# Kernel tuning notes

Measured on AMD Instinct MI355X. Metric: run time of the kernel, lower is better.

## Reference

```python
import jax, jax.numpy as jnp
import numpy as np

BATCH = 16384
IN_F = 1024
OUT_F = 1024
NUM_BASIS = 8
DEGREE = 3
K = NUM_BASIS + DEGREE  # 11 basis columns
EPS = 1e-5


def _knots():
    return jnp.linspace(0.0, 1.0, K + 1)


def _compute_basis(x):
    """Cox-de Boor recursion, faithful to the torch in-place variant:
    at degree d only columns j < K-d are updated; higher columns keep
    their lower-degree values (and are still contracted in the einsum).
    x: [B, IN_F] -> basis: [B, IN_F, K]
    """
    knots = _knots().astype(x.dtype)
    xa = x[..., None]  # [B, IN_F, 1]
    # degree-0 indicator: x in [knots[j], knots[j+1])
    basis = ((xa >= knots[:K]) & (xa < knots[1:K + 1])).astype(x.dtype)
    for d in range(1, DEGREE + 1):
        m = K - d
        denom1 = knots[d:K] - knots[:m]            # [m]
        denom2 = knots[d + 1:K + 1] - knots[1:m + 1]  # [m]
        safe1 = jnp.where(denom1 != 0, denom1, 1.0)
        safe2 = jnp.where(denom2 != 0, denom2, 1.0)
        alpha = jnp.where(denom1 != 0, (xa - knots[:m]) / safe1, 0.0)
        beta = jnp.where(denom2 != 0, (knots[d + 1:K + 1] - xa) / safe2, 0.0)
        new = alpha * basis[..., :m] + beta * basis[..., 1:m + 1]
        basis = jnp.concatenate([new, basis[..., m:]], axis=-1)
    return basis


def setup_inputs() -> dict:
    key = jax.random.key(0)
    k1, k2, k3, k4 = jax.random.split(key, 4)
    x = jax.random.uniform(k1, (BATCH, IN_F), dtype=jnp.float32)
    # Xavier-uniform control points [out, in, K]
    bound_cp = float(np.sqrt(6.0 / (IN_F + K)))  # torch xavier treats last dims as fan
    control_points = jax.random.uniform(k2, (OUT_F, IN_F, K), minval=-bound_cp, maxval=bound_cp, dtype=jnp.float32)
    bound_w = float(np.sqrt(6.0 / (IN_F + OUT_F)))
    W = jax.random.uniform(k3, (OUT_F, IN_F), minval=-bound_w, maxval=bound_w, dtype=jnp.float32)
    b = jnp.zeros((OUT_F,), dtype=jnp.float32)
    gamma = jnp.ones((OUT_F,), dtype=jnp.float32)
    beta = jnp.zeros((OUT_F,), dtype=jnp.float32)
    return {"x": x, "control_points": control_points, "W": W, "b": b,
            "gamma": gamma, "beta": beta}


def reference(x, control_points, W, b, gamma, beta):
    basis = _compute_basis(x)  # [B, IN_F, K]
    spline_out = jnp.einsum('bik,oik->bo', basis, control_points)  # [B, OUT_F]
    out = spline_out + x @ W.T + b
    # LayerNorm over last dim (dropout is identity in eval / p used as 0)
    mu = jnp.mean(out, axis=-1, keepdims=True)
    var = jnp.mean(jnp.square(out - mu), axis=-1, keepdims=True)
    return gamma * (out - mu) * jax.lax.rsqrt(var + EPS) + beta
```

## Files before the change

kernel.cpp:

```cpp
#include <hip/hip_runtime.h>
#include <hip/hip_bf16.h>

#define BATCH   16384
#define IN_F    1024
#define OUT_F   1024
#define KCOLS   11
#define KPL     12
#define KP      (KPL*IN_F)
#define KHALF   (KP/2)
#define NTKH    (KHALF/64)
#define NITH    (NTKH/2)
#define LN_EPS  1e-5f

typedef __attribute__((ext_vector_type(8))) short short8;
typedef __attribute__((ext_vector_type(4))) float f32x4;

static __device__ __forceinline__ unsigned short f2bf(float f) {
  __hip_bfloat16 h = __float2bfloat16(f);
  return *reinterpret_cast<unsigned short*>(&h);
}

__device__ __forceinline__ void bspline_basis(float x, float bas[KCOLS]) {
  const float s = 1.0f / 11.0f;
  float kn[12];
#pragma unroll
  for (int j = 0; j < 12; ++j) kn[j] = (float)j * s;
  kn[11] = 1.0f;
#pragma unroll
  for (int j = 0; j < 11; ++j)
    bas[j] = (x >= kn[j] && x < kn[j + 1]) ? 1.0f : 0.0f;
#pragma unroll
  for (int d = 1; d <= 3; ++d) {
#pragma unroll
    for (int j = 0; j < 11 - d; ++j) {
      const float r1 = 1.0f / (kn[j + d] - kn[j]);
      const float r2 = 1.0f / (kn[j + d + 1] - kn[j + 1]);
      float a = (x - kn[j]) * r1;
      float c = (kn[j + d + 1] - x) * r2;
      bas[j] = a * bas[j] + c * bas[j + 1];
    }
  }
}

__global__ __launch_bounds__(256) void featgen(const float* __restrict__ X,
                                               unsigned short* __restrict__ A,
                                               int row0) {
  const int brow = blockIdx.x;
  const int i0 = threadIdx.x * 4;
  const float4 xv = *reinterpret_cast<const float4*>(X + (size_t)(row0 + brow) * IN_F + i0);
  float xs[4] = {xv.x, xv.y, xv.z, xv.w};
  float bas[4][KCOLS];
#pragma unroll
  for (int t = 0; t < 4; ++t) bspline_basis(xs[t], bas[t]);
  unsigned short* outp = A + (size_t)brow * KP + i0;
#pragma unroll
  for (int k = 0; k < KCOLS; ++k) {
    ushort4 u;
    u.x = f2bf(bas[0][k]); u.y = f2bf(bas[1][k]);
    u.z = f2bf(bas[2][k]); u.w = f2bf(bas[3][k]);
    *reinterpret_cast<ushort4*>(outp + (size_t)k * IN_F) = u;
  }
  ushort4 u;
  u.x = f2bf(xs[0]); u.y = f2bf(xs[1]); u.z = f2bf(xs[2]); u.w = f2bf(xs[3]);
  *reinterpret_cast<ushort4*>(outp + (size_t)KCOLS * IN_F) = u;
}

__global__ __launch_bounds__(256) void bgen(const float* __restrict__ CP,
                                            const float* __restrict__ W,
                                            unsigned short* __restrict__ Bm) {
  const int o = blockIdx.x;
  const int i0 = threadIdx.x * 4;
  unsigned short* outp = Bm + (size_t)o * KP + i0;
#pragma unroll
  for (int k = 0; k < KCOLS; ++k) {
    ushort4 u;
    u.x = f2bf(CP[((size_t)o * IN_F + i0 + 0) * KCOLS + k]);
    u.y = f2bf(CP[((size_t)o * IN_F + i0 + 1) * KCOLS + k]);
    u.z = f2bf(CP[((size_t)o * IN_F + i0 + 2) * KCOLS + k]);
    u.w = f2bf(CP[((size_t)o * IN_F + i0 + 3) * KCOLS + k]);
    *reinterpret_cast<ushort4*>(outp + (size_t)k * IN_F) = u;
  }
  ushort4 u;
  u.x = f2bf(W[(size_t)o * IN_F + i0 + 0]);
  u.y = f2bf(W[(size_t)o * IN_F + i0 + 1]);
  u.z = f2bf(W[(size_t)o * IN_F + i0 + 2]);
  u.w = f2bf(W[(size_t)o * IN_F + i0 + 3]);
  *reinterpret_cast<ushort4*>(outp + (size_t)KCOLS * IN_F) = u;
}


#define BAR()    __builtin_amdgcn_s_barrier()
#define SCHED0() __builtin_amdgcn_sched_barrier(0)
#define WAITV(N) asm volatile("s_waitcnt vmcnt(" #N ")" ::: "memory")

__global__ __launch_bounds__(512, 2) void gemm8p(const unsigned short* __restrict__ A,
                                                 const unsigned short* __restrict__ Bm,
                                                 float* __restrict__ Cc,
                                                 float* __restrict__ Cp, int nbm) {
  __shared__ unsigned short lds[2][2][2][128 * 64];
  const int tid  = (int)threadIdx.x;
  const int lane = tid & 63;
  const int w    = tid >> 6;
  const int wm   = w >> 2;
  const int wn   = w & 3;

  const int nwg = nbm * 8;
  const int cpx = nwg >> 3;
  const int bid = (int)blockIdx.x;
  const int swz = (bid & 7) * cpx + (bid >> 3);
  const int bn = swz & 3;
  const int ks = (swz >> 2) & 1;
  const int bm = swz >> 3;
  const size_t koff = (size_t)ks * KHALF;
  float* __restrict__ C = ks ? Cp : Cc;

  const int srow = (w << 3) + (lane >> 3);
  const int scol = ((lane & 7) ^ (lane >> 3)) << 3;
  const unsigned short* aB = A  + (size_t)(bm * 256 + srow) * KP + koff + scol;
  const unsigned short* bB = Bm + (size_t)(bn * 256 + srow) * KP + koff + scol;

#define STAGE(T, AB, H, BUF)                                                          \
  do {                                                                                \
    if ((T) < NTKH) {                                                                 \
      const unsigned short* g_ = ((AB) ? bB : aB) + (size_t)(H) * 128 * KP + (size_t)(T) * 64; \
      unsigned short* l_ = &lds[BUF][AB][H][w * 512];                                 \
      __builtin_amdgcn_global_load_lds((const __attribute__((address_space(1))) void*)g_,       \
                                       (__attribute__((address_space(3))) void*)l_, 16, 0, 0);  \
      __builtin_amdgcn_global_load_lds((const __attribute__((address_space(1))) void*)(g_ + (size_t)64 * KP), \
                                       (__attribute__((address_space(3))) void*)(l_ + 4096), 16, 0, 0); \
    }                                                                                 \
  } while (0)

  const int fr = lane & 15;
  const int g4 = lane >> 4;
  const int s7 = lane & 7;
  const int col0 = ((g4 ^ s7) << 3);
  const int col1 = (((4 + g4) ^ s7) << 3);
  const unsigned short* aH[2] = {&lds[0][0][wm][0], &lds[1][0][wm][0]};
  const unsigned short* bH[2] = {&lds[0][1][wn >> 1][0], &lds[1][1][wn >> 1][0]};
  const int brow0 = (wn & 1) * 64;

  short8 aF[4][2], bF0[2][2], bF1[2][2];
  f32x4 acc[8][4] = {};

#define LOADA(MB, BUF)                                                         \
  do {                                                                         \
    _Pragma("unroll") for (int m_ = 0; m_ < 4; ++m_) {                         \
      const unsigned short* p_ = aH[BUF] + ((MB) + m_) * 1024 + fr * 64;       \
      aF[m_][0] = *reinterpret_cast<const short8*>(p_ + col0);                 \
      aF[m_][1] = *reinterpret_cast<const short8*>(p_ + col1);                 \
    }                                                                          \
  } while (0)

#define LOADB(DST, NB, BUF)                                                    \
  do {                                                                         \
    _Pragma("unroll") for (int n_ = 0; n_ < 2; ++n_) {                         \
      const unsigned short* p_ = bH[BUF] + (brow0 + ((NB) + n_) * 16 + fr) * 64; \
      DST[n_][0] = *reinterpret_cast<const short8*>(p_ + col0);                \
      DST[n_][1] = *reinterpret_cast<const short8*>(p_ + col1);                \
    }                                                                          \
  } while (0)

#define MFMAQ(MB, NB, BF)                                                      \
  do {                                                                         \
    __builtin_amdgcn_s_setprio(1);                                             \
    _Pragma("unroll") for (int m_ = 0; m_ < 4; ++m_)                           \
    _Pragma("unroll") for (int n_ = 0; n_ < 2; ++n_)                           \
    _Pragma("unroll") for (int kk_ = 0; kk_ < 2; ++kk_)                        \
      acc[(MB) + m_][(NB) + n_] = __builtin_amdgcn_mfma_f32_16x16x32_bf16(     \
          aF[m_][kk_], BF[n_][kk_], acc[(MB) + m_][(NB) + n_], 0, 0, 0);       \
    __builtin_amdgcn_s_setprio(0);                                             \
  } while (0)

  STAGE(0, 1, 0, 0); STAGE(0, 1, 1, 0);
  STAGE(0, 0, 0, 0); STAGE(0, 0, 1, 0);
  STAGE(1, 1, 0, 1); STAGE(1, 1, 1, 1);
  WAITV(4);
  BAR();

#pragma unroll 1
  for (int j = 0; j < NITH; ++j) {
    const int tA = 2 * j + 1, tB2 = 2 * j + 2, tB3 = 2 * j + 3;
    LOADA(0, 0); LOADB(bF0, 0, 0);
    STAGE(tA, 0, 0, 1);
    MFMAQ(0, 0, bF0);
    SCHED0(); BAR();
    LOADB(bF1, 2, 0);
    STAGE(tA, 0, 1, 1);
    MFMAQ(0, 2, bF1);
    SCHED0(); BAR();
    LOADA(4, 0);
    STAGE(tB2, 1, 0, 0);
    MFMAQ(4, 0, bF0);
    SCHED0(); BAR();
    STAGE(tB2, 1, 1, 0);
    MFMAQ(4, 2, bF1);
    if (j < NITH - 1) { WAITV(4); } else { WAITV(0); }
    SCHED0(); BAR();
    LOADA(0, 1); LOADB(bF0, 0, 1);
    STAGE(tB2, 0, 0, 0);
    MFMAQ(0, 0, bF0);
    SCHED0(); BAR();
    LOADB(bF1, 2, 1);
    STAGE(tB2, 0, 1, 0);
    MFMAQ(0, 2, bF1);
    SCHED0(); BAR();
    LOADA(4, 1);
    STAGE(tB3, 1, 0, 1);
    MFMAQ(4, 0, bF0);
    SCHED0(); BAR();
    STAGE(tB3, 1, 1, 1);
    MFMAQ(4, 2, bF1);
    if (j < NITH - 1) { WAITV(4); }
    SCHED0(); BAR();
  }

  const size_t r0 = (size_t)bm * 256 + wm * 128 + (lane >> 4) * 4;
  const int c0 = bn * 256 + wn * 64 + fr;
#pragma unroll
  for (int m = 0; m < 8; ++m)
#pragma unroll
    for (int n = 0; n < 4; ++n)
#pragma unroll
      for (int r = 0; r < 4; ++r)
        C[(r0 + m * 16 + r) * OUT_F + (c0 + n * 16)] = acc[m][n][r];
}

__global__ __launch_bounds__(256) void ln_kernel(float* __restrict__ C,
                                                 const float* __restrict__ P,
                                                 const float* __restrict__ bias,
                                                 const float* __restrict__ gamma,
                                                 const float* __restrict__ beta) {
  const int row = blockIdx.x;
  const int tid = threadIdx.x;
  float4 v = *reinterpret_cast<const float4*>(C + (size_t)row * OUT_F + tid * 4);
  const float4 p = *reinterpret_cast<const float4*>(P + (size_t)row * OUT_F + tid * 4);
  const float4 bb = *reinterpret_cast<const float4*>(bias + tid * 4);
  v.x += p.x + bb.x; v.y += p.y + bb.y; v.z += p.z + bb.z; v.w += p.w + bb.w;
  float s = v.x + v.y + v.z + v.w;
  float q = v.x * v.x + v.y * v.y + v.z * v.z + v.w * v.w;
#pragma unroll
  for (int off = 32; off > 0; off >>= 1) {
    s += __shfl_down(s, off);
    q += __shfl_down(q, off);
  }
  __shared__ float red[8];
  const int wave = tid >> 6, lane = tid & 63;
  if (lane == 0) { red[wave] = s; red[4 + wave] = q; }
  __syncthreads();
  s = red[0] + red[1] + red[2] + red[3];
  q = red[4] + red[5] + red[6] + red[7];
  const float mu = s * (1.0f / OUT_F);
  const float var = q * (1.0f / OUT_F) - mu * mu;
  const float rs = rsqrtf(var + LN_EPS);
  const float4 g = *reinterpret_cast<const float4*>(gamma + tid * 4);
  const float4 be = *reinterpret_cast<const float4*>(beta + tid * 4);
  float4 o;
  o.x = g.x * (v.x - mu) * rs + be.x;
  o.y = g.y * (v.y - mu) * rs + be.y;
  o.z = g.z * (v.z - mu) * rs + be.z;
  o.w = g.w * (v.w - mu) * rs + be.w;
  *reinterpret_cast<float4*>(C + (size_t)row * OUT_F + tid * 4) = o;
}

extern "C" void kernel_launch(void* const* d_in, const int* in_sizes, int n_in,
                              void* d_out, int out_size, void* d_ws, size_t ws_size,
                              hipStream_t stream) {
  const float* x     = (const float*)d_in[0];
  const float* cp    = (const float*)d_in[1];
  const float* W     = (const float*)d_in[2];
  const float* bias  = (const float*)d_in[3];
  const float* gamma = (const float*)d_in[4];
  const float* beta  = (const float*)d_in[5];
  float* out = (float*)d_out;

  unsigned short* Bm = (unsigned short*)d_ws;
  const size_t bBytes = (size_t)OUT_F * KP * sizeof(unsigned short);
  size_t avail = ws_size > bBytes ? ws_size - bBytes : 0;
  const size_t perRow = (size_t)KP * 2 + (size_t)OUT_F * 4;
  long long fit = (long long)(avail / perRow);
  int chunk;
  if (fit >= BATCH)     chunk = BATCH;
  else if (fit >= 8192) chunk = 8192;
  else                  chunk = (int)((fit / 256) * 256);
  if (chunk < 256) chunk = 256;

  unsigned short* Af = (unsigned short*)((char*)d_ws + bBytes);
  float* P = (float*)(Af + (size_t)chunk * KP);

  bgen<<<OUT_F, 256, 0, stream>>>(cp, W, Bm);
  for (int r0 = 0; r0 < BATCH; r0 += chunk) {
    const int rows = (BATCH - r0 < chunk) ? (BATCH - r0) : chunk;
    featgen<<<rows, 256, 0, stream>>>(x, Af, r0);
    const int nbm = rows / 256;
    gemm8p<<<nbm * 8, 512, 0, stream>>>(Af, Bm, out + (size_t)r0 * OUT_F, P, nbm);
    ln_kernel<<<rows, 256, 0, stream>>>(out + (size_t)r0 * OUT_F, P, bias, gamma, beta);
  }
}
```

Measured before the change: 442.3 us.

## Pre-pack B in MFMA fragment order and load it directly from global

The weight/control-point matrix is now packed by a new bgen2 kernel into a layout that matches the per-lane MFMA B-fragment order. The GEMM loads B fragments straight from global memory into registers, so only A is staged through LDS, which halves shared-memory usage and LDS traffic. The cost is more global/L2 reads of B per workgroup with no LDS sharing across waves, and the pipeline wait counts had to be retuned, which may expose load latency.

```diff
diff --git a/kernel.cpp b/kernel.cpp
--- a/kernel.cpp
+++ b/kernel.cpp
@@ -65,27 +65,34 @@
   *reinterpret_cast<ushort4*>(outp + (size_t)KCOLS * IN_F) = u;
 }
 
-__global__ __launch_bounds__(256) void bgen(const float* __restrict__ CP,
-                                            const float* __restrict__ W,
-                                            unsigned short* __restrict__ Bm) {
-  const int o = blockIdx.x;
-  const int i0 = threadIdx.x * 4;
-  unsigned short* outp = Bm + (size_t)o * KP + i0;
-#pragma unroll
-  for (int k = 0; k < KCOLS; ++k) {
-    ushort4 u;
-    u.x = f2bf(CP[((size_t)o * IN_F + i0 + 0) * KCOLS + k]);
-    u.y = f2bf(CP[((size_t)o * IN_F + i0 + 1) * KCOLS + k]);
-    u.z = f2bf(CP[((size_t)o * IN_F + i0 + 2) * KCOLS + k]);
-    u.w = f2bf(CP[((size_t)o * IN_F + i0 + 3) * KCOLS + k]);
-    *reinterpret_cast<ushort4*>(outp + (size_t)k * IN_F) = u;
-  }
-  ushort4 u;
-  u.x = f2bf(W[(size_t)o * IN_F + i0 + 0]);
-  u.y = f2bf(W[(size_t)o * IN_F + i0 + 1]);
-  u.z = f2bf(W[(size_t)o * IN_F + i0 + 2]);
-  u.w = f2bf(W[(size_t)o * IN_F + i0 + 3]);
-  *reinterpret_cast<ushort4*>(outp + (size_t)KCOLS * IN_F) = u;
+__global__ __launch_bounds__(256) void bgen2(const float* __restrict__ CP,
+                                             const float* __restrict__ W,
+                                             unsigned short* __restrict__ BP) {
+  const int bx = blockIdx.x;
+  const int bn = bx / (16 * 96);
+  const int rem = bx % (16 * 96);
+  const int ob = rem / 96;
+  const int tgg = rem % 96;
+  const int tid = threadIdx.x;
+  const int lane = tid & 63;
+  const int kk = (tid >> 6) & 1;
+  const int ts = tid >> 7;
+  const int tg = tgg * 2 + ts;
+  const int fr = lane & 15;
+  const int g4 = lane >> 4;
+  const int o = bn * 256 + ob * 16 + fr;
+  const int k0 = tg * 64 + kk * 32 + g4 * 8;
+  const int p = k0 >> 10;
+  const int i0 = k0 & 1023;
+  unsigned short v[8];
+#pragma unroll
+  for (int e = 0; e < 8; ++e) {
+    float f = (p < KCOLS) ? CP[((size_t)o * IN_F + i0 + e) * KCOLS + p]
+                          : W[(size_t)o * IN_F + i0 + e];
+    v[e] = f2bf(f);
+  }
+  unsigned short* dst = BP + (size_t)tg * 65536 + bn * 16384 + ob * 1024 + kk * 512 + lane * 8;
+  *reinterpret_cast<short8*>(dst) = *reinterpret_cast<short8*>(v);
 }
 
 
@@ -94,10 +101,10 @@
 #define WAITV(N) asm volatile("s_waitcnt vmcnt(" #N ")" ::: "memory")
 
 __global__ __launch_bounds__(512, 2) void gemm8p(const unsigned short* __restrict__ A,
-                                                 const unsigned short* __restrict__ Bm,
+                                                 const unsigned short* __restrict__ BP,
                                                  float* __restrict__ Cc,
                                                  float* __restrict__ Cp, int nbm) {
-  __shared__ unsigned short lds[2][2][2][128 * 64];
+  __shared__ unsigned short lds[2][256 * 64];
   const int tid  = (int)threadIdx.x;
   const int lane = tid & 63;
   const int w    = tid >> 6;
@@ -116,18 +123,14 @@
 
   const int srow = (w << 3) + (lane >> 3);
   const int scol = ((lane & 7) ^ (lane >> 3)) << 3;
-  const unsigned short* aB = A  + (size_t)(bm * 256 + srow) * KP + koff + scol;
-  const unsigned short* bB = Bm + (size_t)(bn * 256 + srow) * KP + koff + scol;
-
-#define STAGE(T, AB, H, BUF)                                                          \
+  const unsigned short* aB = A + (size_t)(bm * 256 + srow) * KP + koff + scol;
+
+#define STAGE_A(T, ISS, BUF)                                                          \
   do {                                                                                \
     if ((T) < NTKH) {                                                                 \
-      const unsigned short* g_ = ((AB) ? bB : aB) + (size_t)(H) * 128 * KP + (size_t)(T) * 64; \
-      unsigned short* l_ = &lds[BUF][AB][H][w * 512];                                 \
-      __builtin_amdgcn_global_load_lds((const __attribute__((address_space(1))) void*)g_,       \
-                                       (__attribute__((address_space(3))) void*)l_, 16, 0, 0);  \
-      __builtin_amdgcn_global_load_lds((const __attribute__((address_space(1))) void*)(g_ + (size_t)64 * KP), \
-                                       (__attribute__((address_space(3))) void*)(l_ + 4096), 16, 0, 0); \
+      const unsigned short* g_ = aB + (size_t)(ISS) * 64 * KP + (size_t)(T) * 64;     \
+      __builtin_amdgcn_global_load_lds((const __attribute__((address_space(1))) void*)g_, \
+          (__attribute__((address_space(3))) void*)(&lds[BUF][(ISS) * 4096 + w * 512]), 16, 0, 0); \
     }                                                                                 \
   } while (0)
 
@@ -136,9 +139,17 @@
   const int s7 = lane & 7;
   const int col0 = ((g4 ^ s7) << 3);
   const int col1 = (((4 + g4) ^ s7) << 3);
-  const unsigned short* aH[2] = {&lds[0][0][wm][0], &lds[1][0][wm][0]};
-  const unsigned short* bH[2] = {&lds[0][1][wn >> 1][0], &lds[1][1][wn >> 1][0]};
-  const int brow0 = (wn & 1) * 64;
+
+  const unsigned short* bpT = BP + (size_t)(ks * NTKH) * 65536 +
+                              (size_t)bn * 16384 + (size_t)wn * 4096 + (size_t)lane * 8;
+
+#define LOADB_G(DST, NB, TG)                                                   \
+  do {                                                                         \
+    const unsigned short* q_ = bpT + (size_t)(TG) * 65536;                     \
+    _Pragma("unroll") for (int n_ = 0; n_ < 2; ++n_)                           \
+    _Pragma("unroll") for (int kk_ = 0; kk_ < 2; ++kk_)                        \
+      DST[n_][kk_] = *reinterpret_cast<const short8*>(q_ + ((NB) + n_) * 1024 + kk_ * 512); \
+  } while (0)
 
   short8 aF[4][2], bF0[2][2], bF1[2][2];
   f32x4 acc[8][4] = {};
@@ -146,18 +157,9 @@
 #define LOADA(MB, BUF)                                                         \
   do {                                                                         \
     _Pragma("unroll") for (int m_ = 0; m_ < 4; ++m_) {                         \
-      const unsigned short* p_ = aH[BUF] + ((MB) + m_) * 1024 + fr * 64;       \
+      const unsigned short* p_ = &lds[BUF][(wm * 128 + ((MB) + m_) * 16 + fr) * 64]; \
       aF[m_][0] = *reinterpret_cast<const short8*>(p_ + col0);                 \
       aF[m_][1] = *reinterpret_cast<const short8*>(p_ + col1);                 \
-    }                                                                          \
-  } while (0)
-
-#define LOADB(DST, NB, BUF)                                                    \
-  do {                                                                         \
-    _Pragma("unroll") for (int n_ = 0; n_ < 2; ++n_) {                         \
-      const unsigned short* p_ = bH[BUF] + (brow0 + ((NB) + n_) * 16 + fr) * 64; \
-      DST[n_][0] = *reinterpret_cast<const short8*>(p_ + col0);                \
-      DST[n_][1] = *reinterpret_cast<const short8*>(p_ + col1);                \
     }                                                                          \
   } while (0)
 
@@ -172,46 +174,49 @@
     __builtin_amdgcn_s_setprio(0);                                             \
   } while (0)
 
-  STAGE(0, 1, 0, 0); STAGE(0, 1, 1, 0);
-  STAGE(0, 0, 0, 0); STAGE(0, 0, 1, 0);
-  STAGE(1, 1, 0, 1); STAGE(1, 1, 1, 1);
-  WAITV(4);
+  STAGE_A(0, 0, 0); STAGE_A(0, 1, 0); STAGE_A(0, 2, 0); STAGE_A(0, 3, 0);
+  STAGE_A(1, 0, 1);
+  LOADB_G(bF0, 0, 0);
+  WAITV(5);
   BAR();
 
 #pragma unroll 1
   for (int j = 0; j < NITH; ++j) {
-    const int tA = 2 * j + 1, tB2 = 2 * j + 2, tB3 = 2 * j + 3;
-    LOADA(0, 0); LOADB(bF0, 0, 0);
-    STAGE(tA, 0, 0, 1);
+    const int ta = 2 * j, tb = 2 * j + 1;
+    const int tgn = (2 * j + 2 < NTKH) ? 2 * j + 2 : NTKH - 1;
+    LOADA(0, 0);
+    LOADB_G(bF1, 2, ta);
+    STAGE_A(tb, 1, 1);
     MFMAQ(0, 0, bF0);
     SCHED0(); BAR();
-    LOADB(bF1, 2, 0);
-    STAGE(tA, 0, 1, 1);
+    STAGE_A(tb, 2, 1);
     MFMAQ(0, 2, bF1);
     SCHED0(); BAR();
     LOADA(4, 0);
-    STAGE(tB2, 1, 0, 0);
+    STAGE_A(tb, 3, 1);
     MFMAQ(4, 0, bF0);
     SCHED0(); BAR();
-    STAGE(tB2, 1, 1, 0);
+    LOADB_G(bF0, 0, tb);
+    STAGE_A(ta + 2, 0, 0);
     MFMAQ(4, 2, bF1);
-    if (j < NITH - 1) { WAITV(4); } else { WAITV(0); }
-    SCHED0(); BAR();
-    LOADA(0, 1); LOADB(bF0, 0, 1);
-    STAGE(tB2, 0, 0, 0);
+    if (j < NITH - 1) { WAITV(5); } else { WAITV(0); }
+    SCHED0(); BAR();
+    LOADA(0, 1);
+    LOADB_G(bF1, 2, tb);
+    STAGE_A(ta + 2, 1, 0);
     MFMAQ(0, 0, bF0);
     SCHED0(); BAR();
-    LOADB(bF1, 2, 1);
-    STAGE(tB2, 0, 1, 0);
+    STAGE_A(ta + 2, 2, 0);
     MFMAQ(0, 2, bF1);
     SCHED0(); BAR();
     LOADA(4, 1);
-    STAGE(tB3, 1, 0, 1);
+    STAGE_A(ta + 2, 3, 0);
     MFMAQ(4, 0, bF0);
     SCHED0(); BAR();
-    STAGE(tB3, 1, 1, 1);
+    LOADB_G(bF0, 0, tgn);
+    STAGE_A(ta + 3, 0, 1);
     MFMAQ(4, 2, bF1);
-    if (j < NITH - 1) { WAITV(4); }
+    if (j < NITH - 1) { WAITV(5); }
     SCHED0(); BAR();
   }
 
@@ -274,7 +279,7 @@
   const float* beta  = (const float*)d_in[5];
   float* out = (float*)d_out;
 
-  unsigned short* Bm = (unsigned short*)d_ws;
+  unsigned short* BP = (unsigned short*)d_ws;
   const size_t bBytes = (size_t)OUT_F * KP * sizeof(unsigned short);
   size_t avail = ws_size > bBytes ? ws_size - bBytes : 0;
   const size_t perRow = (size_t)KP * 2 + (size_t)OUT_F * 4;
@@ -288,12 +293,12 @@
   unsigned short* Af = (unsigned short*)((char*)d_ws + bBytes);
   float* P = (float*)(Af + (size_t)chunk * KP);
 
-  bgen<<<OUT_F, 256, 0, stream>>>(cp, W, Bm);
+  bgen2<<<4 * 16 * 96, 256, 0, stream>>>(cp, W, BP);
   for (int r0 = 0; r0 < BATCH; r0 += chunk) {
     const int rows = (BATCH - r0 < chunk) ? (BATCH - r0) : chunk;
     featgen<<<rows, 256, 0, stream>>>(x, Af, r0);
     const int nbm = rows / 256;
-    gemm8p<<<nbm * 8, 512, 0, stream>>>(Af, Bm, out + (size_t)r0 * OUT_F, P, nbm);
+    gemm8p<<<nbm * 8, 512, 0, stream>>>(Af, BP, out + (size_t)r0 * OUT_F, P, nbm);
     ln_kernel<<<rows, 256, 0, stream>>>(out + (size_t)r0 * OUT_F, P, bias, gamma, beta);
   }
 }
```

Result: slower. 602.5 us (+36.2%).

## Double-buffer A fragments and software-pipeline LDS reads ahead of MFMAs

Applied to the files above, without the earlier changes.

Adds a second register set for A fragments so LDS reads for the next quadrant are issued one phase ahead of the MFMAs that consume them. The main loop's stage and wait ordering changes, with vmcnt waits moved and relaxed from 4 to 2. The aim is to hide LDS read latency behind matrix math. In exchange it uses more VGPRs, which could lower occupancy, and the reordered waits and barriers carry a risk of races on buffer reuse.

```diff
diff --git a/kernel.cpp b/kernel.cpp
--- a/kernel.cpp
+++ b/kernel.cpp
@@ -140,15 +140,15 @@
   const unsigned short* bH[2] = {&lds[0][1][wn >> 1][0], &lds[1][1][wn >> 1][0]};
   const int brow0 = (wn & 1) * 64;
 
-  short8 aF[4][2], bF0[2][2], bF1[2][2];
+  short8 aFA[4][2], aFB[4][2], bF0[2][2], bF1[2][2];
   f32x4 acc[8][4] = {};
 
-#define LOADA(MB, BUF)                                                         \
+#define LOADA_D(DST, MB, BUF)                                                  \
   do {                                                                         \
     _Pragma("unroll") for (int m_ = 0; m_ < 4; ++m_) {                         \
       const unsigned short* p_ = aH[BUF] + ((MB) + m_) * 1024 + fr * 64;       \
-      aF[m_][0] = *reinterpret_cast<const short8*>(p_ + col0);                 \
-      aF[m_][1] = *reinterpret_cast<const short8*>(p_ + col1);                 \
+      DST[m_][0] = *reinterpret_cast<const short8*>(p_ + col0);                \
+      DST[m_][1] = *reinterpret_cast<const short8*>(p_ + col1);                \
     }                                                                          \
   } while (0)
 
@@ -161,57 +161,61 @@
     }                                                                          \
   } while (0)
 
-#define MFMAQ(MB, NB, BF)                                                      \
+#define MFMAQ_D(AFR, MB, NB, BF)                                               \
   do {                                                                         \
     __builtin_amdgcn_s_setprio(1);                                             \
     _Pragma("unroll") for (int m_ = 0; m_ < 4; ++m_)                           \
     _Pragma("unroll") for (int n_ = 0; n_ < 2; ++n_)                           \
     _Pragma("unroll") for (int kk_ = 0; kk_ < 2; ++kk_)                        \
       acc[(MB) + m_][(NB) + n_] = __builtin_amdgcn_mfma_f32_16x16x32_bf16(     \
-          aF[m_][kk_], BF[n_][kk_], acc[(MB) + m_][(NB) + n_], 0, 0, 0);       \
+          AFR[m_][kk_], BF[n_][kk_], acc[(MB) + m_][(NB) + n_], 0, 0, 0);      \
     __builtin_amdgcn_s_setprio(0);                                             \
   } while (0)
 
+  STAGE(0, 0, 0, 0); STAGE(0, 0, 1, 0);
   STAGE(0, 1, 0, 0); STAGE(0, 1, 1, 0);
-  STAGE(0, 0, 0, 0); STAGE(0, 0, 1, 0);
   STAGE(1, 1, 0, 1); STAGE(1, 1, 1, 1);
   WAITV(4);
   BAR();
+  LOADA_D(aFA, 0, 0);
+  LOADB(bF0, 0, 0);
 
 #pragma unroll 1
   for (int j = 0; j < NITH; ++j) {
-    const int tA = 2 * j + 1, tB2 = 2 * j + 2, tB3 = 2 * j + 3;
-    LOADA(0, 0); LOADB(bF0, 0, 0);
-    STAGE(tA, 0, 0, 1);
-    MFMAQ(0, 0, bF0);
-    SCHED0(); BAR();
+    const int tb = 2 * j + 1, t2 = 2 * j + 2, t3 = 2 * j + 3;
     LOADB(bF1, 2, 0);
-    STAGE(tA, 0, 1, 1);
-    MFMAQ(0, 2, bF1);
-    SCHED0(); BAR();
-    LOADA(4, 0);
-    STAGE(tB2, 1, 0, 0);
-    MFMAQ(4, 0, bF0);
-    SCHED0(); BAR();
-    STAGE(tB2, 1, 1, 0);
-    MFMAQ(4, 2, bF1);
-    if (j < NITH - 1) { WAITV(4); } else { WAITV(0); }
-    SCHED0(); BAR();
-    LOADA(0, 1); LOADB(bF0, 0, 1);
-    STAGE(tB2, 0, 0, 0);
-    MFMAQ(0, 0, bF0);
+    STAGE(tb, 0, 0, 1);
+    MFMAQ_D(aFA, 0, 0, bF0);
+    SCHED0(); BAR();
+    LOADA_D(aFB, 4, 0);
+    STAGE(tb, 0, 1, 1);
+    MFMAQ_D(aFA, 0, 2, bF1);
+    SCHED0(); BAR();
+    STAGE(t2, 1, 0, 0);
+    MFMAQ_D(aFB, 4, 0, bF0);
+    if (j < NITH - 1) { WAITV(2); } else { WAITV(0); }
+    SCHED0(); BAR();
+    LOADA_D(aFA, 0, 1);
+    LOADB(bF0, 0, 1);
+    STAGE(t2, 1, 1, 0);
+    MFMAQ_D(aFB, 4, 2, bF1);
     SCHED0(); BAR();
     LOADB(bF1, 2, 1);
-    STAGE(tB2, 0, 1, 0);
-    MFMAQ(0, 2, bF1);
-    SCHED0(); BAR();
-    LOADA(4, 1);
-    STAGE(tB3, 1, 0, 1);
-    MFMAQ(4, 0, bF0);
-    SCHED0(); BAR();
-    STAGE(tB3, 1, 1, 1);
-    MFMAQ(4, 2, bF1);
-    if (j < NITH - 1) { WAITV(4); }
+    STAGE(t2, 0, 0, 0);
+    MFMAQ_D(aFA, 0, 0, bF0);
+    SCHED0(); BAR();
+    LOADA_D(aFB, 4, 1);
+    STAGE(t2, 0, 1, 0);
+    MFMAQ_D(aFA, 0, 2, bF1);
+    SCHED0(); BAR();
+    STAGE(t3, 1, 0, 1);
+    MFMAQ_D(aFB, 4, 0, bF0);
+    if (j < NITH - 1) { WAITV(2); } else { WAITV(0); }
+    SCHED0(); BAR();
+    LOADA_D(aFA, 0, 0);
+    LOADB(bF0, 0, 0);
+    STAGE(t3, 1, 1, 1);
+    MFMAQ_D(aFB, 4, 2, bF1);
     SCHED0(); BAR();
   }
 
```

After: 476.9 us. +7.8%, slower.

## Store split-K GEMM partials as bf16 and widen featgen stores to 16 bytes

Applied to the files above, without the earlier changes.

The GEMM now writes both split-K partial results as bf16 into workspace buffers instead of fp32 into the output and a partial buffer. The LayerNorm kernel reads the two bf16 partials, sums them with the bias and writes fp32 output. This halves partial-result traffic between the GEMM and LayerNorm. Separately, featgen processes 8 features per thread with 16-byte stores, and the GEMM prologue stage order is swapped. The bf16 rounding of the partial sums before normalization reduces accuracy.

```diff
diff --git a/kernel.cpp b/kernel.cpp
--- a/kernel.cpp
+++ b/kernel.cpp
@@ -19,6 +19,10 @@
   __hip_bfloat16 h = __float2bfloat16(f);
   return *reinterpret_cast<unsigned short*>(&h);
 }
+static __device__ __forceinline__ float bf2f(unsigned short u) {
+  unsigned int x = ((unsigned int)u) << 16;
+  return *reinterpret_cast<float*>(&x);
+}
 
 __device__ __forceinline__ void bspline_basis(float x, float bas[KCOLS]) {
   const float s = 1.0f / 11.0f;
@@ -45,24 +49,27 @@
 __global__ __launch_bounds__(256) void featgen(const float* __restrict__ X,
                                                unsigned short* __restrict__ A,
                                                int row0) {
-  const int brow = blockIdx.x;
-  const int i0 = threadIdx.x * 4;
-  const float4 xv = *reinterpret_cast<const float4*>(X + (size_t)(row0 + brow) * IN_F + i0);
-  float xs[4] = {xv.x, xv.y, xv.z, xv.w};
-  float bas[4][KCOLS];
-#pragma unroll
-  for (int t = 0; t < 4; ++t) bspline_basis(xs[t], bas[t]);
+  const int tid = threadIdx.x;
+  const int brow = blockIdx.x * 2 + (tid >> 7);
+  const int i0 = (tid & 127) * 8;
+  const float4 xv0 = *reinterpret_cast<const float4*>(X + (size_t)(row0 + brow) * IN_F + i0);
+  const float4 xv1 = *reinterpret_cast<const float4*>(X + (size_t)(row0 + brow) * IN_F + i0 + 4);
+  float xs[8] = {xv0.x, xv0.y, xv0.z, xv0.w, xv1.x, xv1.y, xv1.z, xv1.w};
+  float bas[8][KCOLS];
+#pragma unroll
+  for (int t = 0; t < 8; ++t) bspline_basis(xs[t], bas[t]);
   unsigned short* outp = A + (size_t)brow * KP + i0;
 #pragma unroll
   for (int k = 0; k < KCOLS; ++k) {
-    ushort4 u;
-    u.x = f2bf(bas[0][k]); u.y = f2bf(bas[1][k]);
-    u.z = f2bf(bas[2][k]); u.w = f2bf(bas[3][k]);
-    *reinterpret_cast<ushort4*>(outp + (size_t)k * IN_F) = u;
-  }
-  ushort4 u;
-  u.x = f2bf(xs[0]); u.y = f2bf(xs[1]); u.z = f2bf(xs[2]); u.w = f2bf(xs[3]);
-  *reinterpret_cast<ushort4*>(outp + (size_t)KCOLS * IN_F) = u;
+    unsigned short u[8];
+#pragma unroll
+    for (int t = 0; t < 8; ++t) u[t] = f2bf(bas[t][k]);
+    *reinterpret_cast<short8*>(outp + (size_t)k * IN_F) = *reinterpret_cast<short8*>(u);
+  }
+  unsigned short u[8];
+#pragma unroll
+  for (int t = 0; t < 8; ++t) u[t] = f2bf(xs[t]);
+  *reinterpret_cast<short8*>(outp + (size_t)KCOLS * IN_F) = *reinterpret_cast<short8*>(u);
 }
 
 __global__ __launch_bounds__(256) void bgen(const float* __restrict__ CP,
@@ -95,8 +102,8 @@
 
 __global__ __launch_bounds__(512, 2) void gemm8p(const unsigned short* __restrict__ A,
                                                  const unsigned short* __restrict__ Bm,
-                                                 float* __restrict__ Cc,
-                                                 float* __restrict__ Cp, int nbm) {
+                                                 unsigned short* __restrict__ Cb0,
+                                                 unsigned short* __restrict__ Cb1, int nbm) {
   __shared__ unsigned short lds[2][2][2][128 * 64];
   const int tid  = (int)threadIdx.x;
   const int lane = tid & 63;
@@ -112,7 +119,7 @@
   const int ks = (swz >> 2) & 1;
   const int bm = swz >> 3;
   const size_t koff = (size_t)ks * KHALF;
-  float* __restrict__ C = ks ? Cp : Cc;
+  unsigned short* __restrict__ C = ks ? Cb1 : Cb0;
 
   const int srow = (w << 3) + (lane >> 3);
   const int scol = ((lane & 7) ^ (lane >> 3)) << 3;
@@ -172,8 +179,8 @@
     __builtin_amdgcn_s_setprio(0);                                             \
   } while (0)
 
+  STAGE(0, 0, 0, 0); STAGE(0, 0, 1, 0);
   STAGE(0, 1, 0, 0); STAGE(0, 1, 1, 0);
-  STAGE(0, 0, 0, 0); STAGE(0, 0, 1, 0);
   STAGE(1, 1, 0, 1); STAGE(1, 1, 1, 1);
   WAITV(4);
   BAR();
@@ -223,20 +230,25 @@
     for (int n = 0; n < 4; ++n)
 #pragma unroll
       for (int r = 0; r < 4; ++r)
-        C[(r0 + m * 16 + r) * OUT_F + (c0 + n * 16)] = acc[m][n][r];
-}
-
-__global__ __launch_bounds__(256) void ln_kernel(float* __restrict__ C,
-                                                 const float* __restrict__ P,
+        C[(r0 + m * 16 + r) * OUT_F + (c0 + n * 16)] = f2bf(acc[m][n][r]);
+}
+
+__global__ __launch_bounds__(256) void ln_kernel(const unsigned short* __restrict__ C0,
+                                                 const unsigned short* __restrict__ C1,
+                                                 float* __restrict__ Out,
                                                  const float* __restrict__ bias,
                                                  const float* __restrict__ gamma,
                                                  const float* __restrict__ beta) {
   const int row = blockIdx.x;
   const int tid = threadIdx.x;
-  float4 v = *reinterpret_cast<const float4*>(C + (size_t)row * OUT_F + tid * 4);
-  const float4 p = *reinterpret_cast<const float4*>(P + (size_t)row * OUT_F + tid * 4);
+  const ushort4 a = *reinterpret_cast<const ushort4*>(C0 + (size_t)row * OUT_F + tid * 4);
+  const ushort4 b = *reinterpret_cast<const ushort4*>(C1 + (size_t)row * OUT_F + tid * 4);
   const float4 bb = *reinterpret_cast<const float4*>(bias + tid * 4);
-  v.x += p.x + bb.x; v.y += p.y + bb.y; v.z += p.z + bb.z; v.w += p.w + bb.w;
+  float4 v;
+  v.x = bf2f(a.x) + bf2f(b.x) + bb.x;
+  v.y = bf2f(a.y) + bf2f(b.y) + bb.y;
+  v.z = bf2f(a.z) + bf2f(b.z) + bb.z;
+  v.w = bf2f(a.w) + bf2f(b.w) + bb.w;
   float s = v.x + v.y + v.z + v.w;
   float q = v.x * v.x + v.y * v.y + v.z * v.z + v.w * v.w;
 #pragma unroll
@@ -260,7 +272,7 @@
   o.y = g.y * (v.y - mu) * rs + be.y;
   o.z = g.z * (v.z - mu) * rs + be.z;
   o.w = g.w * (v.w - mu) * rs + be.w;
-  *reinterpret_cast<float4*>(C + (size_t)row * OUT_F + tid * 4) = o;
+  *reinterpret_cast<float4*>(Out + (size_t)row * OUT_F + tid * 4) = o;
 }
 
 extern "C" void kernel_launch(void* const* d_in, const int* in_sizes, int n_in,
@@ -285,15 +297,17 @@
   else                  chunk = (int)((fit / 256) * 256);
   if (chunk < 256) chunk = 256;
 
-  unsigned short* Af = (unsigned short*)((char*)d_ws + bBytes);
-  float* P = (float*)(Af + (size_t)chunk * KP);
+  unsigned short* Af  = (unsigned short*)((char*)d_ws + bBytes);
+  unsigned short* Cb0 = Af + (size_t)chunk * KP;
+  unsigned short* Cb1 = Cb0 + (size_t)chunk * OUT_F;
 
   bgen<<<OUT_F, 256, 0, stream>>>(cp, W, Bm);
   for (int r0 = 0; r0 < BATCH; r0 += chunk) {
     const int rows = (BATCH - r0 < chunk) ? (BATCH - r0) : chunk;
-    featgen<<<rows, 256, 0, stream>>>(x, Af, r0);
+    featgen<<<rows / 2, 256, 0, stream>>>(x, Af, r0);
     const int nbm = rows / 256;
-    gemm8p<<<nbm * 8, 512, 0, stream>>>(Af, Bm, out + (size_t)r0 * OUT_F, P, nbm);
-    ln_kernel<<<rows, 256, 0, stream>>>(out + (size_t)r0 * OUT_F, P, bias, gamma, beta);
-  }
-}
+    gemm8p<<<nbm * 8, 512, 0, stream>>>(Af, Bm, Cb0, Cb1, nbm);
+    ln_kernel<<<rows, 256, 0, stream>>>(Cb0, Cb1, out + (size_t)r0 * OUT_F,
+                                        bias, gamma, beta);
+  }
+}
```

Result: faster. 432.4 us (-2.2%).
